# Kernel optimization log

Measured on AMD Instinct MI355X. Metric: run time of the kernel, lower is better.

Reference implementation:

```python
import jax, jax.numpy as jnp
import numpy as np

EMBED_DIM = 1024
HID = EMBED_DIM // 2
N = 32768
L2_REG = 0.001
BN_EPS = 1e-5


def setup_inputs() -> dict:
    key = jax.random.key(0)
    ks = jax.random.split(key, 8)
    inp = {
        "item_emb": jax.random.normal(ks[0], (N, EMBED_DIM), jnp.float32),
        "pos_item_emb": jax.random.normal(ks[1], (N, EMBED_DIM), jnp.float32),
        "neg_item_emb": jax.random.normal(ks[2], (N, EMBED_DIM), jnp.float32),
        # Linear 1: embed_dim -> embed_dim/2 (xavier_normal init, zero bias)
        "W1": jax.random.normal(ks[3], (HID, EMBED_DIM), jnp.float32) * np.sqrt(2.0 / (EMBED_DIM + HID)),
        "b1": jnp.zeros((HID,), jnp.float32),
        # BatchNorm1d params / running stats (eval-mode semantics)
        "gamma": jnp.ones((HID,), jnp.float32),
        "beta": jnp.zeros((HID,), jnp.float32),
        "run_mean": jnp.zeros((HID,), jnp.float32),
        "run_var": jnp.ones((HID,), jnp.float32),
        # Linear 2: embed_dim/2 -> embed_dim
        "W2": jax.random.normal(ks[4], (EMBED_DIM, HID), jnp.float32) * np.sqrt(2.0 / (EMBED_DIM + HID)),
        "b2": jnp.zeros((EMBED_DIM,), jnp.float32),
    }
    return inp


def _net(x, W1, b1, gamma, beta, run_mean, run_var, W2, b2):
    # Linear -> BatchNorm1d (eval stats) -> LeakyReLU(0.1) -> (Dropout=identity) -> Linear
    h = x @ W1.T + b1                                   # [N, HID]
    h = (h - run_mean) * jax.lax.rsqrt(run_var + BN_EPS) * gamma + beta
    h = jnp.where(h >= 0, h, 0.1 * h)
    return h @ W2.T + b2                                # [N, EMBED_DIM]


def reference(item_emb, pos_item_emb, neg_item_emb,
              W1, b1, gamma, beta, run_mean, run_var, W2, b2):
    net = lambda x: _net(x, W1, b1, gamma, beta, run_mean, run_var, W2, b2)
    anchor_e = net(item_emb)
    pos_e = net(pos_item_emb)
    neg_e = net(neg_item_emb)

    dist_pos = jnp.linalg.norm(anchor_e - pos_e, axis=1)  # [N]
    dist_neg = jnp.linalg.norm(anchor_e - neg_e, axis=1)  # [N]

    # fused replacement of the per-sample python loop
    margins = jnp.where(dist_neg < dist_pos, dist_pos - dist_neg, 0.0)
    margin = jnp.quantile(margins, 0.25)  # Q1, linear interpolation (matches torch)

    loss_triplet = jax.nn.relu(dist_neg ** 2 - dist_pos ** 2 + margin)
    l2 = L2_REG * (jnp.sum(anchor_e ** 2) + jnp.sum(pos_e ** 2) + jnp.sum(neg_e ** 2)) / anchor_e.shape[0]
    return jnp.mean(loss_triplet + l2)
```

## Files before the change

kernel.cpp:

```cpp
#include <hip/hip_runtime.h>

#define NROWS 32768
#define DIM   1024
#define HIDD  512
#define M3    (3*NROWS)

using bf16x8 = __attribute__((ext_vector_type(8))) short;
using f32x4  = __attribute__((ext_vector_type(4))) float;

#define MFMA16(a,b,c) __builtin_amdgcn_mfma_f32_16x16x32_bf16(a,b,c,0,0,0)
#define WAIT_VM(N)  asm volatile("s_waitcnt vmcnt(" #N ")" ::: "memory")
#define WAIT_LGKM0  asm volatile("s_waitcnt lgkmcnt(0)" ::: "memory")
#define MEMFENCE    asm volatile("" ::: "memory")
#define BAR()       __builtin_amdgcn_s_barrier()
#define SCHEDB()    __builtin_amdgcn_sched_barrier(0)
#define SP1()       __builtin_amdgcn_s_setprio(1)
#define SP0()       __builtin_amdgcn_s_setprio(0)

static __device__ __forceinline__ unsigned short f2bf(float f) {
    unsigned u = __float_as_uint(f);
    u += 0x7FFFu + ((u >> 16) & 1u);
    return (unsigned short)(u >> 16);
}
static __device__ __forceinline__ unsigned cvtpk(float a, float b) {
    unsigned r;
    asm("v_cvt_pk_bf16_f32 %0, %1, %2" : "=v"(r) : "v"(a), "v"(b));
    return r;
}
static __device__ __forceinline__ void gload16(const void* gsrc, void* ldst) {
    __builtin_amdgcn_global_load_lds(
        (const __attribute__((address_space(1))) unsigned int*)gsrc,
        (__attribute__((address_space(3))) unsigned int*)ldst,
        16, 0, 0);
}

__global__ __launch_bounds__(256)
void cvt_kernel(const float* __restrict__ src, unsigned short* __restrict__ dst, int n4)
{
    const int i = blockIdx.x * 256 + threadIdx.x;
    if (i < n4) {
        float4 v = reinterpret_cast<const float4*>(src)[i];
        uint2 o;
        o.x = cvtpk(v.x, v.y);
        o.y = cvtpk(v.z, v.w);
        reinterpret_cast<uint2*>(dst)[i] = o;
    }
}

__global__ __launch_bounds__(256)
void gemm1_mfma(const float* __restrict__ x0, const float* __restrict__ x1,
                const float* __restrict__ x2,
                const unsigned short* __restrict__ W1bf,
                const float* __restrict__ b1, const float* __restrict__ gamma,
                const float* __restrict__ beta, const float* __restrict__ rmean,
                const float* __restrict__ rvar,
                unsigned short* __restrict__ h)
{
    __shared__ unsigned short Abuf[128*64];
    __shared__ unsigned short Bbuf[2*128*32];

    const int lin = blockIdx.x;
    const int wgid = (lin & 7) * 384 + (lin >> 3);
    const int cb = wgid & 3;
    const int rb = wgid >> 2;
    const int tid  = threadIdx.x;
    const int lane = tid & 63, w = tid >> 6;
    const int wr = w >> 1, wc = w & 1;
    const int row0 = rb * 128;
    const int s = row0 >> 15;
    const float* x = (s == 0) ? x0 : (s == 1 ? x1 : x2);
    const int rl0 = row0 & (NROWS - 1);
    const int col0 = cb * 128;
    const int l15 = lane & 15, lq = lane >> 4;

    f32x4 acc[4][4] = {};
    float4 aR[8];

    #pragma unroll
    for (int p = 0; p < 8; ++p) {
        const int f = p * 256 + tid;
        const int r = f >> 4, c4 = f & 15;
        aR[p] = *reinterpret_cast<const float4*>(&x[(size_t)(rl0 + r) * DIM + c4 * 4]);
    }

    for (int t = 0; t < 16; ++t) {
        const int k0 = t * 64;
        #pragma unroll
        for (int p = 0; p < 8; ++p) {
            const int f = p * 256 + tid;
            const int r = f >> 4, c4 = f & 15;
            const unsigned off = (unsigned)((r * 128 + c4 * 8) ^ ((r & 7) << 4));
            uint2 o;
            o.x = cvtpk(aR[p].x, aR[p].y);
            o.y = cvtpk(aR[p].z, aR[p].w);
            *reinterpret_cast<uint2*>(reinterpret_cast<char*>(Abuf) + off) = o;
        }
        #pragma unroll
        for (int c = 0; c < 4; ++c) {
            const int f = c * 256 + tid;
            const int panel = f >> 9;
            const int cc = (f >> 2) & 127;
            const int chunk = (f & 3) ^ ((cc >> 1) & 3);
            gload16(&W1bf[(size_t)(col0 + cc) * DIM + k0 + panel * 32 + chunk * 8],
                    reinterpret_cast<char*>(Bbuf) + (size_t)f * 16);
        }
        __syncthreads();
        if (t < 15) {
            #pragma unroll
            for (int p = 0; p < 8; ++p) {
                const int f = p * 256 + tid;
                const int r = f >> 4, c4 = f & 15;
                aR[p] = *reinterpret_cast<const float4*>(
                    &x[(size_t)(rl0 + r) * DIM + k0 + 64 + c4 * 4]);
            }
        }
        bf16x8 bfv[2][4];
        #pragma unroll
        for (int kk = 0; kk < 2; ++kk)
            #pragma unroll
            for (int n = 0; n < 4; ++n) {
                const int colr = wc*64 + n*16 + l15;
                const int slq = lq ^ ((colr >> 1) & 3);
                bfv[kk][n] = *reinterpret_cast<const bf16x8*>(
                    reinterpret_cast<char*>(Bbuf) + kk*8192 + colr*64 + slq*16);
            }
        #pragma unroll
        for (int kk = 0; kk < 2; ++kk)
            #pragma unroll
            for (int m = 0; m < 4; ++m) {
                const int row = wr*64 + m*16 + l15;
                const unsigned ab = (unsigned)((row*128 + kk*64 + lq*16) ^ ((row & 7) << 4));
                bf16x8 af = *reinterpret_cast<const bf16x8*>(
                    reinterpret_cast<char*>(Abuf) + ab);
                #pragma unroll
                for (int n = 0; n < 4; ++n)
                    acc[m][n] = MFMA16(af, bfv[kk][n], acc[m][n]);
            }
        __syncthreads();
    }

    float As[4], Bsc[4];
    #pragma unroll
    for (int n = 0; n < 4; ++n) {
        const int c = col0 + wc*64 + n*16 + l15;
        const float inv = rsqrtf(rvar[c] + 1e-5f);
        As[n]  = inv * gamma[c];
        Bsc[n] = (b1[c] - rmean[c]) * As[n] + beta[c];
    }
    #pragma unroll
    for (int m = 0; m < 4; ++m) {
        const int rbase = row0 + wr*64 + m*16 + lq*4;
        #pragma unroll
        for (int n = 0; n < 4; ++n) {
            const int c = col0 + wc*64 + n*16 + l15;
            #pragma unroll
            for (int i = 0; i < 4; ++i) {
                float v = fmaf(acc[m][n][i], As[n], Bsc[n]);
                v = (v >= 0.f) ? v : 0.1f * v;
                h[(size_t)(rbase + i) * HIDD + c] = f2bf(v);
            }
        }
    }
}

__global__ __launch_bounds__(512, 1)
void gemm2_mfma(const unsigned short* __restrict__ h,
                const unsigned short* __restrict__ W2bf,
                const float* __restrict__ b2,
                float* __restrict__ pdp, float* __restrict__ pdn,
                float* __restrict__ pl2)
{
    __shared__ char smem[114688];
    char* const Ab = smem;
    char* const Bb = smem + 49152;

    const int lin = blockIdx.x;
    const int wgid = (lin & 7) * 256 + (lin >> 3);
    const int cb = wgid & 3;
    const int rb = wgid >> 2;
    const int tid  = threadIdx.x;
    const int lane = tid & 63, w = tid >> 6;
    const int wm = w >> 2, wn = w & 3;
    const int row0 = rb * 64;
    const int col0 = cb * 256;
    const int l15 = lane & 15, lq = lane >> 4;

    f32x4 acc[6][4] = {};

    auto issueA = [&](int k0, char* Adst) {
        #pragma unroll
        for (int i = 0; i < 3; ++i) {
            const int f = i * 512 + tid;
            const int mrow = f >> 3, c = f & 7;
            const int mf = mrow >> 4, rr = mrow & 15;
            const int ss = mf % 3, rf = mf / 3;
            gload16(&h[((size_t)ss * NROWS + row0 + rf * 16 + rr) * HIDD + k0 + ((c ^ (mrow & 7)) << 3)],
                    Adst + f * 16);
        }
    };
    auto issueB = [&](int k0, char* Bdst) {
        #pragma unroll
        for (int i = 0; i < 4; ++i) {
            const int f = i * 512 + tid;
            const int col = f >> 3, c = f & 7;
            gload16(&W2bf[(size_t)(col0 + col) * HIDD + k0 + ((c ^ (col & 7)) << 3)],
                    Bdst + f * 16);
        }
    };
    auto readA = [&](bf16x8 (&a)[3][2], int mh, char* Abase) {
        #pragma unroll
        for (int mm = 0; mm < 3; ++mm) {
            const int row = (wm * 6 + mh * 3 + mm) * 16 + l15;
            const int swz = (row & 7) << 4;
            #pragma unroll
            for (int ks = 0; ks < 2; ++ks)
                a[mm][ks] = *reinterpret_cast<const bf16x8*>(
                    Abase + ((row * 128 + ks * 64 + lq * 16) ^ swz));
        }
    };
    auto readB = [&](bf16x8 (&b)[2][2], int nh, char* Bbase) {
        #pragma unroll
        for (int nn = 0; nn < 2; ++nn) {
            const int col = wn * 64 + (nh * 2 + nn) * 16 + l15;
            const int swz = (col & 7) << 4;
            #pragma unroll
            for (int ks = 0; ks < 2; ++ks)
                b[nn][ks] = *reinterpret_cast<const bf16x8*>(
                    Bbase + ((col * 128 + ks * 64 + lq * 16) ^ swz));
        }
    };

    issueA(0, Ab);
    MEMFENCE;
    issueB(0, Bb);
    WAIT_VM(0);
    BAR();

    for (int t = 0; t < 8; ++t) {
        char* const Apt = Ab + (t & 1) * 24576;
        char* const Apn = Ab + ((t & 1) ^ 1) * 24576;
        char* const Bpt = Bb + (t & 1) * 32768;
        char* const Bpn = Bb + ((t & 1) ^ 1) * 32768;
        const int kn = ((t < 7) ? (t + 1) : 7) * 64;

        bf16x8 a[3][2], b[2][2], a2[3][2];
        readA(a, 0, Apt);
        readB(b, 0, Bpt);
        issueA(kn, Apn);
        MEMFENCE;
        issueB(kn, Bpn);
        BAR(); WAIT_LGKM0; SCHEDB(); SP1();
        #pragma unroll
        for (int mm = 0; mm < 3; ++mm)
            #pragma unroll
            for (int nn = 0; nn < 2; ++nn)
                #pragma unroll
                for (int ks = 0; ks < 2; ++ks)
                    acc[mm][nn] = MFMA16(a[mm][ks], b[nn][ks], acc[mm][nn]);
        SP0(); BAR();
        readB(b, 1, Bpt);
        BAR(); WAIT_LGKM0; SCHEDB(); SP1();
        #pragma unroll
        for (int mm = 0; mm < 3; ++mm)
            #pragma unroll
            for (int nn = 0; nn < 2; ++nn)
                #pragma unroll
                for (int ks = 0; ks < 2; ++ks)
                    acc[mm][2 + nn] = MFMA16(a[mm][ks], b[nn][ks], acc[mm][2 + nn]);
        SP0(); BAR();
        readA(a2, 1, Apt);
        BAR(); WAIT_LGKM0; SCHEDB(); SP1();
        #pragma unroll
        for (int mm = 0; mm < 3; ++mm)
            #pragma unroll
            for (int nn = 0; nn < 2; ++nn)
                #pragma unroll
                for (int ks = 0; ks < 2; ++ks)
                    acc[3 + mm][2 + nn] = MFMA16(a2[mm][ks], b[nn][ks], acc[3 + mm][2 + nn]);
        SP0(); BAR();
        readB(b, 0, Bpt);
        WAIT_VM(0);
        BAR(); WAIT_LGKM0; SCHEDB(); SP1();
        #pragma unroll
        for (int mm = 0; mm < 3; ++mm)
            #pragma unroll
            for (int nn = 0; nn < 2; ++nn)
                #pragma unroll
                for (int ks = 0; ks < 2; ++ks)
                    acc[3 + mm][nn] = MFMA16(a2[mm][ks], b[nn][ks], acc[3 + mm][nn]);
        SP0(); BAR();
    }

    float b2c[4];
    #pragma unroll
    for (int nf = 0; nf < 4; ++nf) b2c[nf] = b2[col0 + wn * 64 + nf * 16 + l15];
    float l2t = 0.f;
    #pragma unroll
    for (int mh = 0; mh < 2; ++mh) {
        const int rbase = row0 + (wm * 2 + mh) * 16 + lq * 4;
        #pragma unroll
        for (int i = 0; i < 4; ++i) {
            float dp = 0.f, dn = 0.f;
            #pragma unroll
            for (int nf = 0; nf < 4; ++nf) {
                const float ea = acc[mh * 3 + 0][nf][i] + b2c[nf];
                const float ep = acc[mh * 3 + 1][nf][i] + b2c[nf];
                const float en = acc[mh * 3 + 2][nf][i] + b2c[nf];
                dp += (ea - ep) * (ea - ep);
                dn += (ea - en) * (ea - en);
                l2t += ea * ea + ep * ep + en * en;
            }
            #pragma unroll
            for (int mm = 1; mm < 16; mm <<= 1) {
                dp += __shfl_xor(dp, mm);
                dn += __shfl_xor(dn, mm);
            }
            if (l15 == 0) {
                pdp[(size_t)(cb * 4 + wn) * NROWS + rbase + i] = dp;
                pdn[(size_t)(cb * 4 + wn) * NROWS + rbase + i] = dn;
            }
        }
    }
    #pragma unroll
    for (int mm = 1; mm < 64; mm <<= 1) l2t += __shfl_xor(l2t, mm);
    __syncthreads();
    float* const l2red = (float*)smem;
    if (lane == 0) l2red[w] = l2t;
    __syncthreads();
    if (tid == 0) {
        float t = 0.f;
        #pragma unroll
        for (int ww = 0; ww < 8; ++ww) t += l2red[ww];
        pl2[wgid] = t;
    }
}

__global__ __launch_bounds__(256)
void margins_kernel(const float* __restrict__ pdp, const float* __restrict__ pdn,
                    float* __restrict__ margins, float* __restrict__ dd)
{
    const int r = blockIdx.x * 256 + threadIdx.x;
    float dp2 = 0.f, dn2 = 0.f;
    #pragma unroll
    for (int q = 0; q < 16; ++q) {
        dp2 += pdp[(size_t)q * NROWS + r];
        dn2 += pdn[(size_t)q * NROWS + r];
    }
    dd[r] = dn2 - dp2;
    margins[r] = (dn2 < dp2) ? (sqrtf(dp2) - sqrtf(dn2)) : 0.f;
}

__global__ __launch_bounds__(1024)
void final_kernel(const float* __restrict__ pl2, int npl2,
                  const float* __restrict__ margins, const float* __restrict__ dd,
                  float* __restrict__ out)
{
    __shared__ unsigned hist[256];
    __shared__ float warp_red[16];
    __shared__ unsigned wsum[4];
    __shared__ unsigned sh_prefix;
    __shared__ int sh_k;
    __shared__ float sh_l2;
    __shared__ unsigned sh_cle;
    __shared__ unsigned sh_minAbove;
    const int tid = threadIdx.x;

    float l2 = 0.f;
    for (int i = tid; i < npl2; i += 1024) l2 += pl2[i];
    #pragma unroll
    for (int m = 1; m < 64; m <<= 1) l2 += __shfl_xor(l2, m);
    if ((tid & 63) == 0) warp_red[tid >> 6] = l2;
    __syncthreads();
    if (tid == 0) {
        float t = 0.f;
        for (int w = 0; w < 16; ++w) t += warp_red[w];
        sh_l2 = t;
        sh_k = 8191; sh_prefix = 0u;
        sh_cle = 0u; sh_minAbove = 0xFFFFFFFFu;
    }
    __syncthreads();

    for (int shift = 24; shift >= 0; shift -= 8) {
        if (tid < 256) hist[tid] = 0u;
        __syncthreads();
        const unsigned prefix = sh_prefix;
        const int kcur = sh_k;
        const unsigned mask = (shift == 24) ? 0u : (0xFFFFFFFFu << (shift + 8));
        for (int i = tid; i < NROWS; i += 1024) {
            const unsigned key = __float_as_uint(margins[i]);
            if (((key ^ prefix) & mask) == 0u)
                atomicAdd(&hist[(key >> shift) & 255u], 1u);
        }
        __syncthreads();
        unsigned v = 0, cme = 0;
        if (tid < 256) {
            cme = hist[tid];
            v = cme;
            #pragma unroll
            for (int off = 1; off < 64; off <<= 1) {
                unsigned tt = __shfl_up(v, off);
                if ((tid & 63) >= off) v += tt;
            }
            if ((tid & 63) == 63) wsum[tid >> 6] = v;
        }
        __syncthreads();
        if (tid < 256) {
            unsigned wo = 0;
            for (int i = 0; i < (tid >> 6); ++i) wo += wsum[i];
            const unsigned incl = v + wo;
            const unsigned excl = incl - cme;
            if ((unsigned)kcur >= excl && (unsigned)kcur < incl) {
                sh_prefix = prefix | ((unsigned)tid << shift);
                sh_k = kcur - (int)excl;
            }
        }
        __syncthreads();
    }
    const unsigned p1u = sh_prefix;

    unsigned lc = 0, lmin = 0xFFFFFFFFu;
    for (int i = tid; i < NROWS; i += 1024) {
        const unsigned key = __float_as_uint(margins[i]);
        if (key <= p1u) ++lc; else lmin = min(lmin, key);
    }
    #pragma unroll
    for (int m = 1; m < 64; m <<= 1) {
        lc += __shfl_xor(lc, m);
        lmin = min(lmin, (unsigned)__shfl_xor((int)lmin, m));
    }
    if ((tid & 63) == 0) {
        atomicAdd(&sh_cle, lc);
        atomicMin(&sh_minAbove, lmin);
    }
    __syncthreads();
    const float p1 = __uint_as_float(p1u);
    const float p2 = (sh_cle >= 8193u) ? p1 : __uint_as_float(sh_minAbove);
    const float margin = p1 + 0.75f * (p2 - p1);

    float ssum = 0.f;
    for (int i = tid; i < NROWS; i += 1024) {
        const float t = dd[i] + margin;
        ssum += (t > 0.f) ? t : 0.f;
    }
    #pragma unroll
    for (int m = 1; m < 64; m <<= 1) ssum += __shfl_xor(ssum, m);
    if ((tid & 63) == 0) warp_red[tid >> 6] = ssum;
    __syncthreads();
    if (tid == 0) {
        float S = 0.f;
        for (int w = 0; w < 16; ++w) S += warp_red[w];
        out[0] = S / (float)NROWS + 1e-3f * sh_l2 / (float)NROWS;
    }
}

extern "C" void kernel_launch(void* const* d_in, const int* in_sizes, int n_in,
                              void* d_out, int out_size, void* d_ws, size_t ws_size,
                              hipStream_t stream) {
    (void)in_sizes; (void)n_in; (void)out_size; (void)ws_size;
    const float* item = (const float*)d_in[0];
    const float* pos  = (const float*)d_in[1];
    const float* neg  = (const float*)d_in[2];
    const float* W1   = (const float*)d_in[3];
    const float* b1   = (const float*)d_in[4];
    const float* gam  = (const float*)d_in[5];
    const float* bet  = (const float*)d_in[6];
    const float* rmu  = (const float*)d_in[7];
    const float* rvr  = (const float*)d_in[8];
    const float* W2   = (const float*)d_in[9];
    const float* b2   = (const float*)d_in[10];

    char* ws = (char*)d_ws;
    unsigned short* h = (unsigned short*)ws;
    size_t off = (size_t)M3 * HIDD * sizeof(unsigned short);
    unsigned short* W1bf = (unsigned short*)(ws + off); off += (size_t)HIDD * DIM * 2;
    unsigned short* W2bf = (unsigned short*)(ws + off); off += (size_t)DIM * HIDD * 2;
    float* pdp = (float*)(ws + off); off += (size_t)16 * NROWS * 4;
    float* pdn = (float*)(ws + off); off += (size_t)16 * NROWS * 4;
    float* pl2 = (float*)(ws + off); off += (size_t)2048 * 4;
    float* margins = (float*)(ws + off); off += (size_t)NROWS * 4;
    float* dd = (float*)(ws + off); off += (size_t)NROWS * 4;

    cvt_kernel<<<dim3((HIDD*DIM/4 + 255)/256), 256, 0, stream>>>(W1, W1bf, HIDD*DIM/4);
    cvt_kernel<<<dim3((DIM*HIDD/4 + 255)/256), 256, 0, stream>>>(W2, W2bf, DIM*HIDD/4);
    gemm1_mfma<<<dim3(3072), 256, 0, stream>>>(
        item, pos, neg, W1bf, b1, gam, bet, rmu, rvr, h);
    gemm2_mfma<<<dim3(2048), 512, 0, stream>>>(
        h, W2bf, b2, pdp, pdn, pl2);
    margins_kernel<<<dim3(NROWS/256), 256, 0, stream>>>(pdp, pdn, margins, dd);
    final_kernel<<<1, 1024, 0, stream>>>(pl2, 2048, margins, dd, (float*)d_out);
}
```

Baseline: 422.6 us.

## Replace second GEMM with Gram-matrix formulation to halve output width

Precomputes G = W2^T W2 and W2^T b2, so the second GEMM outputs 512 columns instead of 1024. Distances and L2 norms are then recovered as inner products of G·h with h, which is reloaded in the epilogue. This roughly halves the MFMA work and W2 traffic of the dominant kernel. In exchange it adds a small FP32 Gram kernel, an extra epilogue load of h, and bf16 rounding of G, which can make squared distances slightly negative; these are clamped.

```diff
diff --git a/kernel.cpp b/kernel.cpp
--- a/kernel.cpp
+++ b/kernel.cpp
@@ -22,6 +22,9 @@
     u += 0x7FFFu + ((u >> 16) & 1u);
     return (unsigned short)(u >> 16);
 }
+static __device__ __forceinline__ float bf2f(unsigned short s) {
+    return __uint_as_float(((unsigned)s) << 16);
+}
 static __device__ __forceinline__ unsigned cvtpk(float a, float b) {
     unsigned r;
     asm("v_cvt_pk_bf16_f32 %0, %1, %2" : "=v"(r) : "v"(a), "v"(b));
@@ -45,6 +48,47 @@
         o.y = cvtpk(v.z, v.w);
         reinterpret_cast<uint2*>(dst)[i] = o;
     }
+}
+
+__global__ __launch_bounds__(256)
+void gram_kernel(const float* __restrict__ W2, unsigned short* __restrict__ Gbf)
+{
+    __shared__ float Wi[32][32];
+    __shared__ float Wj[32][32];
+    const int i0 = blockIdx.x * 32, j0 = blockIdx.y * 32;
+    const int tid = threadIdx.x;
+    const int kq = tid >> 3, c4 = (tid & 7) * 4;
+    const int ti = (tid & 15) * 2, tj = (tid >> 4) * 2;
+    float s00 = 0.f, s01 = 0.f, s10 = 0.f, s11 = 0.f;
+    for (int k0 = 0; k0 < DIM; k0 += 32) {
+        *reinterpret_cast<float4*>(&Wi[kq][c4]) =
+            *reinterpret_cast<const float4*>(&W2[(size_t)(k0 + kq) * HIDD + i0 + c4]);
+        *reinterpret_cast<float4*>(&Wj[kq][c4]) =
+            *reinterpret_cast<const float4*>(&W2[(size_t)(k0 + kq) * HIDD + j0 + c4]);
+        __syncthreads();
+        #pragma unroll
+        for (int k = 0; k < 32; ++k) {
+            const float2 a = *reinterpret_cast<const float2*>(&Wi[k][ti]);
+            const float2 b = *reinterpret_cast<const float2*>(&Wj[k][tj]);
+            s00 = fmaf(a.x, b.x, s00); s01 = fmaf(a.x, b.y, s01);
+            s10 = fmaf(a.y, b.x, s10); s11 = fmaf(a.y, b.y, s11);
+        }
+        __syncthreads();
+    }
+    *reinterpret_cast<unsigned*>(&Gbf[(size_t)(i0 + ti) * HIDD + j0 + tj])     = cvtpk(s00, s01);
+    *reinterpret_cast<unsigned*>(&Gbf[(size_t)(i0 + ti + 1) * HIDD + j0 + tj]) = cvtpk(s10, s11);
+}
+
+__global__ __launch_bounds__(64)
+void w2b_kernel(const float* __restrict__ W2, const float* __restrict__ b2,
+                float* __restrict__ w2b)
+{
+    const int c = blockIdx.x * 64 + threadIdx.x;
+    const int m0 = blockIdx.y * 256;
+    float acc = 0.f;
+    for (int m = m0; m < m0 + 256; ++m)
+        acc = fmaf(W2[(size_t)m * HIDD + c], b2[m], acc);
+    atomicAdd(&w2b[c], acc);
 }
 
 __global__ __launch_bounds__(256)
@@ -165,12 +209,12 @@
 
 __global__ __launch_bounds__(512, 1)
 void gemm2_mfma(const unsigned short* __restrict__ h,
-                const unsigned short* __restrict__ W2bf,
-                const float* __restrict__ b2,
+                const unsigned short* __restrict__ Gbf,
+                const float* __restrict__ w2b,
                 float* __restrict__ pdp, float* __restrict__ pdn,
                 float* __restrict__ pl2)
 {
-    __shared__ char smem[114688];
+    __shared__ char smem[81920];
     char* const Ab = smem;
     char* const Bb = smem + 49152;
 
@@ -182,10 +226,10 @@
     const int lane = tid & 63, w = tid >> 6;
     const int wm = w >> 2, wn = w & 3;
     const int row0 = rb * 64;
-    const int col0 = cb * 256;
+    const int col0 = cb * 128;
     const int l15 = lane & 15, lq = lane >> 4;
 
-    f32x4 acc[6][4] = {};
+    f32x4 acc[6][2] = {};
 
     auto issueA = [&](int k0, char* Adst) {
         #pragma unroll
@@ -200,10 +244,10 @@
     };
     auto issueB = [&](int k0, char* Bdst) {
         #pragma unroll
-        for (int i = 0; i < 4; ++i) {
+        for (int i = 0; i < 2; ++i) {
             const int f = i * 512 + tid;
             const int col = f >> 3, c = f & 7;
-            gload16(&W2bf[(size_t)(col0 + col) * HIDD + k0 + ((c ^ (col & 7)) << 3)],
+            gload16(&Gbf[(size_t)(col0 + col) * HIDD + k0 + ((c ^ (col & 7)) << 3)],
                     Bdst + f * 16);
         }
     };
@@ -218,16 +262,13 @@
                     Abase + ((row * 128 + ks * 64 + lq * 16) ^ swz));
         }
     };
-    auto readB = [&](bf16x8 (&b)[2][2], int nh, char* Bbase) {
-        #pragma unroll
-        for (int nn = 0; nn < 2; ++nn) {
-            const int col = wn * 64 + (nh * 2 + nn) * 16 + l15;
-            const int swz = (col & 7) << 4;
-            #pragma unroll
-            for (int ks = 0; ks < 2; ++ks)
-                b[nn][ks] = *reinterpret_cast<const bf16x8*>(
-                    Bbase + ((col * 128 + ks * 64 + lq * 16) ^ swz));
-        }
+    auto readB = [&](bf16x8 (&b)[2], int nh, char* Bbase) {
+        const int col = wn * 32 + nh * 16 + l15;
+        const int swz = (col & 7) << 4;
+        #pragma unroll
+        for (int ks = 0; ks < 2; ++ks)
+            b[ks] = *reinterpret_cast<const bf16x8*>(
+                Bbase + ((col * 128 + ks * 64 + lq * 16) ^ swz));
     };
 
     issueA(0, Ab);
@@ -239,11 +280,11 @@
     for (int t = 0; t < 8; ++t) {
         char* const Apt = Ab + (t & 1) * 24576;
         char* const Apn = Ab + ((t & 1) ^ 1) * 24576;
-        char* const Bpt = Bb + (t & 1) * 32768;
-        char* const Bpn = Bb + ((t & 1) ^ 1) * 32768;
+        char* const Bpt = Bb + (t & 1) * 16384;
+        char* const Bpn = Bb + ((t & 1) ^ 1) * 16384;
         const int kn = ((t < 7) ? (t + 1) : 7) * 64;
 
-        bf16x8 a[3][2], b[2][2], a2[3][2];
+        bf16x8 a[3][2], b[2], a2[3][2];
         readA(a, 0, Apt);
         readB(b, 0, Bpt);
         issueA(kn, Apn);
@@ -253,30 +294,24 @@
         #pragma unroll
         for (int mm = 0; mm < 3; ++mm)
             #pragma unroll
-            for (int nn = 0; nn < 2; ++nn)
-                #pragma unroll
-                for (int ks = 0; ks < 2; ++ks)
-                    acc[mm][nn] = MFMA16(a[mm][ks], b[nn][ks], acc[mm][nn]);
+            for (int ks = 0; ks < 2; ++ks)
+                acc[mm][0] = MFMA16(a[mm][ks], b[ks], acc[mm][0]);
         SP0(); BAR();
         readB(b, 1, Bpt);
         BAR(); WAIT_LGKM0; SCHEDB(); SP1();
         #pragma unroll
         for (int mm = 0; mm < 3; ++mm)
             #pragma unroll
-            for (int nn = 0; nn < 2; ++nn)
-                #pragma unroll
-                for (int ks = 0; ks < 2; ++ks)
-                    acc[mm][2 + nn] = MFMA16(a[mm][ks], b[nn][ks], acc[mm][2 + nn]);
+            for (int ks = 0; ks < 2; ++ks)
+                acc[mm][1] = MFMA16(a[mm][ks], b[ks], acc[mm][1]);
         SP0(); BAR();
         readA(a2, 1, Apt);
         BAR(); WAIT_LGKM0; SCHEDB(); SP1();
         #pragma unroll
         for (int mm = 0; mm < 3; ++mm)
             #pragma unroll
-            for (int nn = 0; nn < 2; ++nn)
-                #pragma unroll
-                for (int ks = 0; ks < 2; ++ks)
-                    acc[3 + mm][2 + nn] = MFMA16(a2[mm][ks], b[nn][ks], acc[3 + mm][2 + nn]);
+            for (int ks = 0; ks < 2; ++ks)
+                acc[3 + mm][1] = MFMA16(a2[mm][ks], b[ks], acc[3 + mm][1]);
         SP0(); BAR();
         readB(b, 0, Bpt);
         WAIT_VM(0);
@@ -284,31 +319,49 @@
         #pragma unroll
         for (int mm = 0; mm < 3; ++mm)
             #pragma unroll
-            for (int nn = 0; nn < 2; ++nn)
-                #pragma unroll
-                for (int ks = 0; ks < 2; ++ks)
-                    acc[3 + mm][nn] = MFMA16(a2[mm][ks], b[nn][ks], acc[3 + mm][nn]);
+            for (int ks = 0; ks < 2; ++ks)
+                acc[3 + mm][0] = MFMA16(a2[mm][ks], b[ks], acc[3 + mm][0]);
         SP0(); BAR();
     }
 
-    float b2c[4];
-    #pragma unroll
-    for (int nf = 0; nf < 4; ++nf) b2c[nf] = b2[col0 + wn * 64 + nf * 16 + l15];
+    uint4 hv[6]; int hoff[6];
+    #pragma unroll
+    for (int i = 0; i < 6; ++i) {
+        const int f = i * 512 + tid;
+        const int ss = f >> 10, rem = f & 1023, r = rem >> 4, c16 = rem & 15;
+        hv[i] = *reinterpret_cast<const uint4*>(
+            &h[((size_t)ss * NROWS + row0 + r) * HIDD + col0 + c16 * 8]);
+        hoff[i] = ss * 17408 + r * 272 + c16 * 16;
+    }
+    __syncthreads();
+    #pragma unroll
+    for (int i = 0; i < 6; ++i)
+        *reinterpret_cast<uint4*>(smem + hoff[i]) = hv[i];
+    __syncthreads();
+
+    float w2b2[2];
+    w2b2[0] = 2.f * w2b[col0 + wn * 32 + l15];
+    w2b2[1] = 2.f * w2b[col0 + wn * 32 + 16 + l15];
     float l2t = 0.f;
     #pragma unroll
     for (int mh = 0; mh < 2; ++mh) {
-        const int rbase = row0 + (wm * 2 + mh) * 16 + lq * 4;
         #pragma unroll
         for (int i = 0; i < 4; ++i) {
+            const int r_loc = (wm * 2 + mh) * 16 + lq * 4 + i;
             float dp = 0.f, dn = 0.f;
             #pragma unroll
-            for (int nf = 0; nf < 4; ++nf) {
-                const float ea = acc[mh * 3 + 0][nf][i] + b2c[nf];
-                const float ep = acc[mh * 3 + 1][nf][i] + b2c[nf];
-                const float en = acc[mh * 3 + 2][nf][i] + b2c[nf];
-                dp += (ea - ep) * (ea - ep);
-                dn += (ea - en) * (ea - en);
-                l2t += ea * ea + ep * ep + en * en;
+            for (int nf = 0; nf < 2; ++nf) {
+                const int c_loc = wn * 32 + nf * 16 + l15;
+                const int hb = r_loc * 272 + c_loc * 2;
+                const float ha = bf2f(*reinterpret_cast<const unsigned short*>(smem + hb));
+                const float hp = bf2f(*reinterpret_cast<const unsigned short*>(smem + 17408 + hb));
+                const float hn = bf2f(*reinterpret_cast<const unsigned short*>(smem + 34816 + hb));
+                const float ua = acc[mh * 3 + 0][nf][i];
+                const float up = acc[mh * 3 + 1][nf][i];
+                const float un = acc[mh * 3 + 2][nf][i];
+                dp += (ua - up) * (ha - hp);
+                dn += (ua - un) * (ha - hn);
+                l2t += (ua + w2b2[nf]) * ha + (up + w2b2[nf]) * hp + (un + w2b2[nf]) * hn;
             }
             #pragma unroll
             for (int mm = 1; mm < 16; mm <<= 1) {
@@ -316,15 +369,14 @@
                 dn += __shfl_xor(dn, mm);
             }
             if (l15 == 0) {
-                pdp[(size_t)(cb * 4 + wn) * NROWS + rbase + i] = dp;
-                pdn[(size_t)(cb * 4 + wn) * NROWS + rbase + i] = dn;
+                pdp[(size_t)(cb * 4 + wn) * NROWS + row0 + r_loc] = dp;
+                pdn[(size_t)(cb * 4 + wn) * NROWS + row0 + r_loc] = dn;
             }
         }
     }
     #pragma unroll
     for (int mm = 1; mm < 64; mm <<= 1) l2t += __shfl_xor(l2t, mm);
-    __syncthreads();
-    float* const l2red = (float*)smem;
+    float* const l2red = (float*)(smem + 53248);
     if (lane == 0) l2red[w] = l2t;
     __syncthreads();
     if (tid == 0) {
@@ -346,12 +398,15 @@
         dp2 += pdp[(size_t)q * NROWS + r];
         dn2 += pdn[(size_t)q * NROWS + r];
     }
+    dp2 = fmaxf(dp2, 0.f);
+    dn2 = fmaxf(dn2, 0.f);
     dd[r] = dn2 - dp2;
     margins[r] = (dn2 < dp2) ? (sqrtf(dp2) - sqrtf(dn2)) : 0.f;
 }
 
 __global__ __launch_bounds__(1024)
 void final_kernel(const float* __restrict__ pl2, int npl2,
+                  const float* __restrict__ b2,
                   const float* __restrict__ margins, const float* __restrict__ dd,
                   float* __restrict__ out)
 {
@@ -365,7 +420,8 @@
     __shared__ unsigned sh_minAbove;
     const int tid = threadIdx.x;
 
-    float l2 = 0.f;
+    const float bb = b2[tid];
+    float l2 = 3.0f * (float)NROWS * bb * bb;
     for (int i = tid; i < npl2; i += 1024) l2 += pl2[i];
     #pragma unroll
     for (int m = 1; m < 64; m <<= 1) l2 += __shfl_xor(l2, m);
@@ -473,19 +529,22 @@
     unsigned short* h = (unsigned short*)ws;
     size_t off = (size_t)M3 * HIDD * sizeof(unsigned short);
     unsigned short* W1bf = (unsigned short*)(ws + off); off += (size_t)HIDD * DIM * 2;
-    unsigned short* W2bf = (unsigned short*)(ws + off); off += (size_t)DIM * HIDD * 2;
+    unsigned short* Gbf  = (unsigned short*)(ws + off); off += (size_t)HIDD * HIDD * 2;
+    float* w2b = (float*)(ws + off); off += (size_t)HIDD * 4;
     float* pdp = (float*)(ws + off); off += (size_t)16 * NROWS * 4;
     float* pdn = (float*)(ws + off); off += (size_t)16 * NROWS * 4;
     float* pl2 = (float*)(ws + off); off += (size_t)2048 * 4;
     float* margins = (float*)(ws + off); off += (size_t)NROWS * 4;
     float* dd = (float*)(ws + off); off += (size_t)NROWS * 4;
 
+    hipMemsetAsync(w2b, 0, HIDD * sizeof(float), stream);
     cvt_kernel<<<dim3((HIDD*DIM/4 + 255)/256), 256, 0, stream>>>(W1, W1bf, HIDD*DIM/4);
-    cvt_kernel<<<dim3((DIM*HIDD/4 + 255)/256), 256, 0, stream>>>(W2, W2bf, DIM*HIDD/4);
+    gram_kernel<<<dim3(16, 16), 256, 0, stream>>>(W2, Gbf);
+    w2b_kernel<<<dim3(8, 4), 64, 0, stream>>>(W2, b2, w2b);
     gemm1_mfma<<<dim3(3072), 256, 0, stream>>>(
         item, pos, neg, W1bf, b1, gam, bet, rmu, rvr, h);
     gemm2_mfma<<<dim3(2048), 512, 0, stream>>>(
-        h, W2bf, b2, pdp, pdn, pl2);
+        h, Gbf, w2b, pdp, pdn, pl2);
     margins_kernel<<<dim3(NROWS/256), 256, 0, stream>>>(pdp, pdn, margins, dd);
-    final_kernel<<<1, 1024, 0, stream>>>(pl2, 2048, margins, dd, (float*)d_out);
-}
+    final_kernel<<<1, 1024, 0, stream>>>(pl2, 2048, b2, margins, dd, (float*)d_out);
+}
```

New measurement: 478.2 us. 1.13x slower.
